# Optimization experiments

Measured on AMD Instinct MI355X. Metric: run time of the kernel, lower is better.

The kernel has to match this reference:

```python
import jax, jax.numpy as jnp
import numpy as np
from jax import lax


def ternarize(w):
    """Standard TWN ternarization with straight-through estimator.
    delta = 0.7*mean(|w|); alpha = mean(|w|) over kept entries; w_t = alpha*sign(w)*mask.
    """
    a = jnp.abs(w)
    delta = 0.7 * a.mean()
    mask = (a > delta).astype(w.dtype)
    alpha = (a * mask).sum() / jnp.maximum(mask.sum(), 1.0)
    wt = alpha * jnp.sign(w) * mask
    return w + lax.stop_gradient(wt - w)  # STE


def conv3x3(x, w, b):
    y = lax.conv_general_dilated(x, ternarize(w), window_strides=(1, 1),
                                 padding=((1, 1), (1, 1)),
                                 dimension_numbers=('NCHW', 'OIHW', 'NCHW'))
    return y + b[None, :, None, None]


def maxpool2(x):
    return lax.reduce_window(x, -jnp.inf, lax.max, (1, 1, 2, 2), (1, 1, 2, 2), 'VALID')


def setup_inputs() -> dict:
    key = jax.random.key(0)
    ks = jax.random.split(key, 11)
    s = lambda k, shape, scale: jax.random.normal(k, shape, dtype=jnp.float32) * scale
    return {
        'x':   s(ks[0], (1024, 3, 32, 32), 1.0),
        'w1':  s(ks[1], (64, 3, 3, 3), 0.1),
        'b1':  s(ks[2], (64,), 0.01),
        'w2':  s(ks[3], (128, 64, 3, 3), 0.05),
        'b2':  s(ks[4], (128,), 0.01),
        'w3':  s(ks[5], (256, 128, 3, 3), 0.03),
        'b3':  s(ks[6], (256,), 0.01),
        'wf1': s(ks[7], (256, 4096), 0.02),
        'bf1': s(ks[8], (256,), 0.01),
        'wf2': s(ks[9], (10, 256), 0.06),
        'bf2': s(ks[10], (10,), 0.01),
    }


def reference(x, w1, b1, w2, b2, w3, b3, wf1, bf1, wf2, bf2):
    x = maxpool2(jax.nn.relu(conv3x3(x, w1, b1)))   # [B,64,16,16]
    x = maxpool2(jax.nn.relu(conv3x3(x, w2, b2)))   # [B,128,8,8]
    x = maxpool2(jax.nn.relu(conv3x3(x, w3, b3)))   # [B,256,4,4]
    x = x.reshape(-1, 256 * 4 * 4)
    x = jax.nn.relu(x @ ternarize(wf1).T + bf1)     # [B,256]
    return x @ ternarize(wf2).T + bf2               # [B,10]
```

## Files before the change

kernel.cpp:

```cpp
#include <hip/hip_runtime.h>
#include <hip/hip_bf16.h>


typedef __attribute__((ext_vector_type(8))) short short8;
typedef __attribute__((ext_vector_type(4))) float f32x4;
typedef __attribute__((ext_vector_type(4))) int i32x4;

__device__ __forceinline__ unsigned short f2bf(float x) {
    unsigned u = __float_as_uint(x);
    return (unsigned short)((u + 0x7fffu + ((u >> 16) & 1u)) >> 16);
}
__device__ __forceinline__ float bf2f(unsigned short b) {
    return __uint_as_float(((unsigned)b) << 16);
}

#define WS_W1B   0
#define N_W1B    2048
#define WS_W2P   (WS_W1B + N_W1B)
#define N_W2P    (9*128*64)
#define WS_W3P   (WS_W2P + N_W2P)
#define N_W3P    (9*256*128)
#define WS_WTF1  (WS_W3P + N_W3P)
#define N_WTF1   (256*4096)
#define WS_WTF2  (WS_WTF1 + N_WTF1)
#define N_WTF2   (10*256)
#define WS_A1    (WS_WTF2 + N_WTF2)
#define N_A1     (1024*256*64)
#define WS_A2    (WS_A1 + N_A1)
#define N_A2     (1024*64*128)
#define WS_A3    (WS_A2 + N_A2)
#define N_A3     (1024*16*256)
#define WS_F1    (WS_A3 + N_A3)
#define N_F1     (1024*256)
#define WS_SCR   (WS_F1 + N_F1)

#define FC1_S    16

struct TernArgs {
    const float* w[6];
    int n[6];
};

__global__ void tern_stats1(TernArgs ta, double* __restrict__ scr) {
    const int wi = blockIdx.y;
    const float* __restrict__ w = ta.w[wi];
    const int n = ta.n[wi];
    __shared__ double red[4];
    const int lane = threadIdx.x & 63, wv = threadIdx.x >> 6;
    if (wi == 5) {
        float m = 0.f;
        for (int i = blockIdx.x * blockDim.x + threadIdx.x; i < n;
             i += gridDim.x * blockDim.x)
            m = fmaxf(m, fabsf(w[i]));
        #pragma unroll
        for (int off = 32; off > 0; off >>= 1)
            m = fmaxf(m, __shfl_down(m, off, 64));
        if (lane == 0) red[wv] = (double)m;
        __syncthreads();
        if (threadIdx.x == 0) {
            float mm = (float)fmax(fmax(red[0], red[1]), fmax(red[2], red[3]));
            atomicMax((int*)(scr + 20), __float_as_int(mm));
        }
        return;
    }
    double s = 0.0;
    for (int i = blockIdx.x * blockDim.x + threadIdx.x; i < n;
         i += gridDim.x * blockDim.x)
        s += (double)fabsf(w[i]);
    #pragma unroll
    for (int off = 32; off > 0; off >>= 1) s += __shfl_down(s, off, 64);
    if (lane == 0) red[wv] = s;
    __syncthreads();
    if (threadIdx.x == 0)
        atomicAdd(scr + wi * 4, red[0] + red[1] + red[2] + red[3]);
}

__global__ void tern_stats2(TernArgs ta, double* __restrict__ scr) {
    const int wi = blockIdx.y;
    const float* __restrict__ w = ta.w[wi];
    const int n = ta.n[wi];
    const float delta = (float)(0.7 * scr[wi * 4] / (double)n);
    double ms = 0.0, cnt = 0.0;
    for (int i = blockIdx.x * blockDim.x + threadIdx.x; i < n;
         i += gridDim.x * blockDim.x) {
        float a = fabsf(w[i]);
        if (a > delta) { ms += (double)a; cnt += 1.0; }
    }
    #pragma unroll
    for (int off = 32; off > 0; off >>= 1) {
        ms += __shfl_down(ms, off, 64);
        cnt += __shfl_down(cnt, off, 64);
    }
    __shared__ double redm[4], redc[4];
    const int lane = threadIdx.x & 63, wv = threadIdx.x >> 6;
    if (lane == 0) { redm[wv] = ms; redc[wv] = cnt; }
    __syncthreads();
    if (threadIdx.x == 0) {
        atomicAdd(scr + wi * 4 + 1, redm[0] + redm[1] + redm[2] + redm[3]);
        atomicAdd(scr + wi * 4 + 2, redc[0] + redc[1] + redc[2] + redc[3]);
    }
}

__global__ void tern_write_all(TernArgs ta, const double* __restrict__ scr,
                               signed char* __restrict__ w1b,
                               signed char* __restrict__ w2p8,
                               signed char* __restrict__ w3p8,
                               unsigned short* __restrict__ wtf1b,
                               float* __restrict__ wtf2) {
    const int wi = blockIdx.y;
    const float* __restrict__ w = ta.w[wi];
    const int n = ta.n[wi];
    const double* sc = scr + wi * 4;
    const float delta = (float)(0.7 * sc[0] / (double)n);
    const int i0 = blockIdx.x * blockDim.x + threadIdx.x;
    const int stride = gridDim.x * blockDim.x;

    if (wi == 0) {
        for (int i = i0; i < n; i += stride) {
            const int co = i / 27;
            const int kp = i % 27;
            float v = w[i];
            signed char s = (fabsf(v) > delta) ? (v > 0.0f ? 1 : -1) : 0;
            w1b[co * 64 + kp] = s;
            w1b[4096 + co * 64 + 32 + kp] = s;
        }
    } else if (wi == 4) {
        const double c = sc[2];
        const float alpha = (float)(sc[1] / (c > 1.0 ? c : 1.0));
        for (int i = i0; i < n; i += stride) {
            float v = w[i];
            wtf2[i] = (fabsf(v) > delta) ? (v > 0.0f ? alpha : -alpha) : 0.0f;
        }
    } else if (wi == 1 || wi == 2) {
        const int CIc = (wi == 1) ? 64 : 128;
        const int COc = (wi == 1) ? 128 : 256;
        signed char* dst = (wi == 1) ? w2p8 : w3p8;
        for (int i = i0; i < n; i += stride) {
            const int co = i / (CIc * 9);
            const int r = i % (CIc * 9);
            const int ci = r / 9, tap = r % 9;
            float v = w[i];
            signed char s = (fabsf(v) > delta) ? (v > 0.0f ? 1 : -1) : 0;
            dst[(tap * COc + co) * CIc + ci] = s;
        }
    } else {
        for (int i = i0; i < n; i += stride) {
            const int j = i >> 12;
            const int k = i & 4095;
            const int c = k >> 4, px = k & 15;
            float v = w[i];
            unsigned short s = (fabsf(v) > delta) ? (v > 0.0f ? 0x3f80 : 0xbf80) : 0;
            unsigned short* row = wtf1b + ((long)j << 13) + px * 512 + c;
            row[0] = s;
            row[256] = s;
        }
    }
}

__global__ __launch_bounds__(256) void conv1_i8(
        const float* __restrict__ x,
        const signed char* __restrict__ w1b,
        const float* __restrict__ bias,
        const double* __restrict__ scr,
        const int* __restrict__ amax_x,
        int* __restrict__ amax_out,
        float* __restrict__ y) {
    constexpr int PL = 3472;
    __shared__ __align__(16) char X[2 * PL];
    __shared__ float redm[4];

    const int b = blockIdx.x;
    const int tid = threadIdx.x;
    const float S = 32512.0f / fmaxf(__int_as_float(*amax_x), 1e-30f);

    for (int i = tid; i < 2 * PL / 16; i += 256)
        ((int4*)X)[i] = make_int4(0, 0, 0, 0);
    __syncthreads();

    for (int i = tid; i < 768; i += 256) {
        const float4 v = ((const float4*)(x + (long)b * 3072))[i];
        const int e = i * 4;
        const int ci = e >> 10;
        const int rem = e & 1023;
        const int h = rem >> 5, w = rem & 31;
        const int base = ci * 1156 + (h + 1) * 34 + (w + 1);
        const float f[4] = {v.x, v.y, v.z, v.w};
        #pragma unroll
        for (int j = 0; j < 4; j++) {
            const int q = __float2int_rn(f[j] * S);
            const int ql = (q << 24) >> 24;
            const int qh = (q - ql) >> 8;
            X[base + j] = (char)ql;
            X[PL + base + j] = (char)qh;
        }
    }
    __syncthreads();

    const int lane = tid & 63;
    const int wid = tid >> 6;
    const int lm = lane & 15;
    const int kg = lane >> 4;

    const int poff = (kg >= 2) ? PL : 0;
    int cst[16];
    #pragma unroll
    for (int j = 0; j < 16; j++) {
        const int kp = (kg & 1) * 16 + j;
        cst[j] = (kp < 27)
                     ? ((kp / 9) * 1156 + ((kp % 9) / 3) * 34 + (kp % 9) % 3)
                     : 0;
    }

    i32x4 BL[4], BH[4];
    #pragma unroll
    for (int nt = 0; nt < 4; nt++) {
        const int co = nt * 16 + lm;
        BL[nt] = *(const i32x4*)(w1b + (long)co * 64 + kg * 16);
        BH[nt] = *(const i32x4*)(w1b + 4096 + (long)co * 64 + kg * 16);
    }

    const double c2 = scr[2];
    const float alpha = (float)(scr[1] / (c2 > 1.0 ? c2 : 1.0));
    const float dq = alpha / S;
    float tmax = 0.f;
    float* yb = y + (long)b * 256 * 64;

    for (int tt = 0; tt < 16; ++tt) {
        const int t = wid * 16 + tt;
        const int pp = t * 4 + (lm >> 2);
        const int sub = lm & 3;
        const int h = 2 * (pp >> 4) + (sub >> 1);
        const int w = 2 * (pp & 15) + (sub & 1);
        const int base = poff + h * 34 + w;
        unsigned d[4] = {0u, 0u, 0u, 0u};
        #pragma unroll
        for (int j = 0; j < 16; j++) {
            const unsigned byte = (unsigned char)X[base + cst[j]];
            d[j >> 2] |= byte << ((j & 3) * 8);
        }
        i32x4 Af;
        Af[0] = (int)d[0]; Af[1] = (int)d[1];
        Af[2] = (int)d[2]; Af[3] = (int)d[3];

        const int opp = t * 4 + kg;
        float* yr = yb + (long)opp * 64;
        #pragma unroll
        for (int nt = 0; nt < 4; nt++) {
            i32x4 aL = 0, aH = 0;
            aL = __builtin_amdgcn_mfma_i32_16x16x64_i8(Af, BL[nt], aL, 0, 0, 0);
            aH = __builtin_amdgcn_mfma_i32_16x16x64_i8(Af, BH[nt], aH, 0, 0, 0);
            const int s0 = aH[0] * 256 + aL[0];
            const int s1 = aH[1] * 256 + aL[1];
            const int s2 = aH[2] * 256 + aL[2];
            const int s3 = aH[3] * 256 + aL[3];
            int sm = s0 > s1 ? s0 : s1;
            const int sn = s2 > s3 ? s2 : s3;
            sm = sm > sn ? sm : sn;
            const int co = nt * 16 + lm;
            const float o = fmaxf(dq * (float)sm + bias[co], 0.f);
            tmax = fmaxf(tmax, o);
            yr[co] = o;
        }
    }

    #pragma unroll
    for (int off = 32; off > 0; off >>= 1)
        tmax = fmaxf(tmax, __shfl_down(tmax, off, 64));
    if (lane == 0) redm[wid] = tmax;
    __syncthreads();
    if (tid == 0) {
        float m = fmaxf(fmaxf(redm[0], redm[1]), fmaxf(redm[2], redm[3]));
        atomicMax(amax_out, __float_as_int(m));
    }
}

template <int CI, int HI, int CO, int HB, int WM, int WN, bool INF32>
__global__ __launch_bounds__(256) void conv_i8(
        const void* __restrict__ xin,
        const signed char* __restrict__ wp,
        const float* __restrict__ bias,
        const double* __restrict__ scr,
        const int* __restrict__ amax_in,
        int* __restrict__ amax_out,
        unsigned short* __restrict__ yout) {
    constexpr int CH8 = CI / 64;
    constexpr int NITER = 9 * CH8;
    constexpr int HR = HI / HB;
    constexpr int ROWS = HR + 2;
    constexpr int COLS = HI + 2;
    constexpr int NPIX = ROWS * COLS;
    constexpr int PSTR = NPIX * 64 + 32;
    constexpr int PO = HI / 2;
    constexpr int POR = HR / 2;
    constexpr int MT = 4, NT = 4;
    constexpr int NST = ROWS * HI * (CI / 8) / 256;
    static_assert(WM * WN == 4, "4 waves");
    static_assert(WM * 64 == HR * HI, "M covers slab pixels");
    static_assert(WN * 64 == CO, "N covers all co");
    static_assert(NST * 256 == ROWS * HI * (CI / 8), "exact staging trips");

    __shared__ __align__(16) char X[2 * CH8 * PSTR];
    __shared__ float redm[4];

    const int bimg = blockIdx.x / HB;
    const int hb = blockIdx.x % HB;
    const int tid = threadIdx.x;

    const float S = 32512.0f / fmaxf(__int_as_float(*amax_in), 1e-30f);

    constexpr int HALO = 2 * COLS + 2 * (ROWS - 2);
    for (int i = tid; i < HALO * 2 * CH8 * 4; i += 256) {
        const int u = i & 3;
        const int t = i >> 2;
        const int g = t % (2 * CH8);
        const int hp = t / (2 * CH8);
        int p;
        if (hp < COLS) p = hp;
        else if (hp < 2 * COLS) p = (ROWS - 1) * COLS + (hp - COLS);
        else {
            const int e = hp - 2 * COLS;
            p = (1 + (e >> 1)) * COLS + ((e & 1) ? (COLS - 1) : 0);
        }
        *(int4*)&X[g * PSTR + p * 64 + u * 16] = make_int4(0, 0, 0, 0);
    }

    uint4 va[NST], vb[NST];
    bool val[NST];
    int pidx[NST], cbase[NST];
    #pragma unroll
    for (int s2 = 0; s2 < NST; s2++) {
        const int i = tid + s2 * 256;
        const int q8 = i % (CI / 8);
        const int t = i / (CI / 8);
        const int c = t % HI;
        const int r = t / HI;
        const int h = hb * HR + r - 1;
        val[s2] = (unsigned)h < (unsigned)HI;
        pidx[s2] = r * COLS + c + 1;
        cbase[s2] = q8 * 8;
        if (val[s2]) {
            if (INF32) {
                const float* pxr = (const float*)xin +
                    ((long)(bimg * HI + h) * HI + c) * CI + q8 * 8;
                va[s2] = *(const uint4*)(pxr);
                vb[s2] = *(const uint4*)(pxr + 4);
            } else {
                const unsigned short* pxr = (const unsigned short*)xin +
                    ((long)(bimg * HI + h) * HI + c) * (2 * CI);
                va[s2] = *(const uint4*)(pxr + q8 * 8);
                vb[s2] = *(const uint4*)(pxr + CI + q8 * 8);
            }
        }
    }
    #pragma unroll
    for (int s2 = 0; s2 < NST; s2++) {
        if (!val[s2]) continue;
        float f[8];
        if (INF32) {
            const float* fa = (const float*)&va[s2];
            const float* fb = (const float*)&vb[s2];
            #pragma unroll
            for (int j = 0; j < 4; j++) { f[j] = fa[j]; f[4 + j] = fb[j]; }
        } else {
            const unsigned* hw = (const unsigned*)&va[s2];
            const unsigned* lw = (const unsigned*)&vb[s2];
            #pragma unroll
            for (int j = 0; j < 8; j++) {
                const unsigned hu = (j & 1) ? (hw[j >> 1] >> 16)
                                            : (hw[j >> 1] & 0xffffu);
                const unsigned lu = (j & 1) ? (lw[j >> 1] >> 16)
                                            : (lw[j >> 1] & 0xffffu);
                f[j] = __uint_as_float(hu << 16) + __uint_as_float(lu << 16);
            }
        }
        unsigned pl0 = 0, pl1 = 0, ph0 = 0, ph1 = 0;
        #pragma unroll
        for (int j = 0; j < 8; j++) {
            const int qi = (int)(f[j] * S + 0.5f);
            const int ql = (qi << 24) >> 24;
            const int qh = (qi - ql) >> 8;
            const int sh = (j & 3) * 8;
            if (j < 4) {
                pl0 |= (unsigned)(ql & 255) << sh;
                ph0 |= (unsigned)(qh & 255) << sh;
            } else {
                pl1 |= (unsigned)(ql & 255) << sh;
                ph1 |= (unsigned)(qh & 255) << sh;
            }
        }
        const int p = pidx[s2];
        const int ch = cbase[s2] >> 6;
        const int cc = cbase[s2] & 63;
        const int slot = ((cc >> 4) + (p >> 1)) & 3;
        const int base = p * 64 + slot * 16 + (cc & 15);
        *(uint2*)&X[ch * PSTR + base] = make_uint2(pl0, pl1);
        *(uint2*)&X[(CH8 + ch) * PSTR + base] = make_uint2(ph0, ph1);
    }
    __syncthreads();

    const int lane = tid & 63;
    const int wid = tid >> 6;
    const int wm = (WM == 1) ? 0 : (wid >> 1);
    const int wn = (WM == 1) ? wid : (wid & 1);
    const int lm = lane & 15;
    const int kg = lane >> 4;

    int pb[MT];
    #pragma unroll
    for (int mt = 0; mt < MT; mt++) {
        const int m = (wm * MT + mt) * 16 + lm;
        const int pp = m >> 2, sub = m & 3;
        const int lph = pp / PO, lpw = pp % PO;
        const int h = 2 * lph + (sub >> 1);
        const int w = 2 * lpw + (sub & 1);
        pb[mt] = h * COLS + w;
    }
    const signed char* bp[NT];
    #pragma unroll
    for (int nt = 0; nt < NT; nt++) {
        const int co = (wn * NT + nt) * 16 + lm;
        bp[nt] = wp + (long)co * CI + kg * 16;
    }

    i32x4 accL[MT][NT], accH[MT][NT];
    #pragma unroll
    for (int mt = 0; mt < MT; mt++)
        #pragma unroll
        for (int nt = 0; nt < NT; nt++) { accL[mt][nt] = 0; accH[mt][nt] = 0; }

    i32x4 Bb[2][NT];
    #pragma unroll
    for (int nt = 0; nt < NT; nt++) Bb[0][nt] = *(const i32x4*)(bp[nt]);

    #pragma unroll 2
    for (int it = 0; it < NITER; ++it) {
        const int cur = it & 1, nxt = cur ^ 1;
        if (it + 1 < NITER) {
            const int it1 = it + 1;
            const int tap = it1 / CH8, ch1 = it1 % CH8;
            const int woff = tap * CO * CI + ch1 * 64;
            #pragma unroll
            for (int nt = 0; nt < NT; nt++)
                Bb[nxt][nt] = *(const i32x4*)(bp[nt] + woff);
        }
        const int tap = it / CH8, ch = it % CH8;
        const int dtap = (tap / 3) * COLS + (tap % 3);
        i32x4 Af0[MT], Af1[MT];
        #pragma unroll
        for (int mt = 0; mt < MT; mt++) {
            const int p = pb[mt] + dtap;
            const int ao = p * 64 + (((kg + (p >> 1)) & 3) << 4);
            Af0[mt] = *(const i32x4*)&X[ch * PSTR + ao];
            Af1[mt] = *(const i32x4*)&X[(CH8 + ch) * PSTR + ao];
        }
        #pragma unroll
        for (int mt = 0; mt < MT; mt++)
            #pragma unroll
            for (int nt = 0; nt < NT; nt++)
                accL[mt][nt] = __builtin_amdgcn_mfma_i32_16x16x64_i8(
                    Af0[mt], Bb[cur][nt], accL[mt][nt], 0, 0, 0);
        #pragma unroll
        for (int mt = 0; mt < MT; mt++)
            #pragma unroll
            for (int nt = 0; nt < NT; nt++)
                accH[mt][nt] = __builtin_amdgcn_mfma_i32_16x16x64_i8(
                    Af1[mt], Bb[cur][nt], accH[mt][nt], 0, 0, 0);
    }

    const double c2 = scr[2];
    const float alpha = (float)(scr[1] / (c2 > 1.0 ? c2 : 1.0));
    const float dq = alpha / S;
    float tmax = 0.f;
    #pragma unroll
    for (int mt = 0; mt < MT; mt++) {
        const int pp = (wm * MT + mt) * 4 + kg;
        const int lph = pp / PO, lpw = pp % PO;
        const int gpp = (hb * POR + lph) * PO + lpw;
        unsigned short* yr = yout + ((long)bimg * (PO * PO) + gpp) * (2 * CO);
        #pragma unroll
        for (int nt = 0; nt < NT; nt++) {
            const int co = (wn * NT + nt) * 16 + lm;
            const i32x4 aL = accL[mt][nt], aH = accH[mt][nt];
            int s0 = aH[0] * 256 + aL[0];
            int s1 = aH[1] * 256 + aL[1];
            int s2 = aH[2] * 256 + aL[2];
            int s3 = aH[3] * 256 + aL[3];
            int sm = s0 > s1 ? s0 : s1;
            int sn = s2 > s3 ? s2 : s3;
            sm = sm > sn ? sm : sn;
            float o = fmaxf(dq * (float)sm + bias[co], 0.f);
            tmax = fmaxf(tmax, o);
            unsigned short hi = f2bf(o);
            unsigned short lo = f2bf(o - bf2f(hi));
            yr[co] = hi;
            yr[CO + co] = lo;
        }
    }
    if (amax_out) {
        #pragma unroll
        for (int off = 32; off > 0; off >>= 1)
            tmax = fmaxf(tmax, __shfl_down(tmax, off, 64));
        if (lane == 0) redm[wid] = tmax;
        __syncthreads();
        if (tid == 0) {
            float m = fmaxf(fmaxf(redm[0], redm[1]), fmaxf(redm[2], redm[3]));
            atomicMax(amax_out, __float_as_int(m));
        }
    }
}

template <int S>
__global__ __launch_bounds__(256) void fc1_mfma(
        const unsigned short* __restrict__ A,
        const unsigned short* __restrict__ Bw,
        float* __restrict__ parts) {
    constexpr int KCH = 8192 / S;
    constexpr int NSTEP = KCH / 32;
    const int m0 = blockIdx.x * 128;
    const int n0 = blockIdx.y * 128;
    const int s = blockIdx.z;
    const int tid = threadIdx.x;
    const int lane = tid & 63, wid = tid >> 6;
    const int wm = wid >> 1, wn = wid & 1;
    const int lm = lane & 15, kg = lane >> 4;

    const long k0 = (long)s * KCH + kg * 8;
    const unsigned short* ap[4];
    const unsigned short* bp[4];
    #pragma unroll
    for (int t = 0; t < 4; t++) {
        ap[t] = A + (long)(m0 + wm * 64 + t * 16 + lm) * 8192 + k0;
        bp[t] = Bw + (long)(n0 + wn * 64 + t * 16 + lm) * 8192 + k0;
    }

    f32x4 acc[4][4] = {};
    short8 Ab[2][4], Bb[2][4];
    #pragma unroll
    for (int t = 0; t < 4; t++) {
        Ab[0][t] = *(const short8*)(ap[t]);
        Bb[0][t] = *(const short8*)(bp[t]);
    }

    #pragma unroll 2
    for (int st = 0; st < NSTEP; ++st) {
        const int cur = st & 1, nxt = cur ^ 1;
        if (st + 1 < NSTEP) {
            const int off = (st + 1) * 32;
            #pragma unroll
            for (int t = 0; t < 4; t++) {
                Ab[nxt][t] = *(const short8*)(ap[t] + off);
                Bb[nxt][t] = *(const short8*)(bp[t] + off);
            }
        }
        #pragma unroll
        for (int mt = 0; mt < 4; mt++)
            #pragma unroll
            for (int nt = 0; nt < 4; nt++)
                acc[mt][nt] = __builtin_amdgcn_mfma_f32_16x16x32_bf16(
                    Ab[cur][mt], Bb[cur][nt], acc[mt][nt], 0, 0, 0);
    }

    #pragma unroll
    for (int mt = 0; mt < 4; mt++) {
        #pragma unroll
        for (int r = 0; r < 4; r++) {
            const int b = m0 + wm * 64 + mt * 16 + kg * 4 + r;
            #pragma unroll
            for (int nt = 0; nt < 4; nt++) {
                const int j = n0 + wn * 64 + nt * 16 + lm;
                parts[((long)s * 1024 + b) * 256 + j] = acc[mt][nt][r];
            }
        }
    }
}

template <int S>
__global__ void fc1_reduce(const float* __restrict__ parts,
                           const double* __restrict__ scr,
                           const float* __restrict__ bias,
                           float* __restrict__ f1) {
    const int idx = blockIdx.x * blockDim.x + threadIdx.x;
    const int j = idx & 255;
    float s = 0.f;
    #pragma unroll
    for (int p = 0; p < S; p++) s += parts[(long)p * 262144 + idx];
    const double c2 = scr[2];
    const float alpha = (float)(scr[1] / (c2 > 1.0 ? c2 : 1.0));
    f1[idx] = fmaxf(alpha * s + bias[j], 0.f);
}

__global__ void fc2_kernel(const float* __restrict__ a,
                           const float* __restrict__ wt,
                           const float* __restrict__ bias,
                           float* __restrict__ out, int B) {
    const int idx = blockIdx.x * blockDim.x + threadIdx.x;
    if (idx >= B * 10) return;
    const int k = idx % 10;
    const int b = idx / 10;
    const float* ar = a + (long)b * 256;
    const float* wr = wt + (long)k * 256;
    float acc = 0.f;
    #pragma unroll 4
    for (int i = 0; i < 256; i++) acc += ar[i] * wr[i];
    out[idx] = acc + bias[k];
}

extern "C" void kernel_launch(void* const* d_in, const int* in_sizes, int n_in,
                              void* d_out, int out_size, void* d_ws, size_t ws_size,
                              hipStream_t stream) {
    const float* x   = (const float*)d_in[0];
    const float* w1  = (const float*)d_in[1];
    const float* b1  = (const float*)d_in[2];
    const float* w2  = (const float*)d_in[3];
    const float* b2  = (const float*)d_in[4];
    const float* w3  = (const float*)d_in[5];
    const float* b3  = (const float*)d_in[6];
    const float* wf1 = (const float*)d_in[7];
    const float* bf1 = (const float*)d_in[8];
    const float* wf2 = (const float*)d_in[9];
    const float* bf2 = (const float*)d_in[10];
    float* out = (float*)d_out;
    float* ws = (float*)d_ws;

    const int B = 1024;

    signed char*    w1b   = (signed char*)(ws + WS_W1B);
    signed char*    w2p8  = (signed char*)(ws + WS_W2P);
    signed char*    w3p8  = (signed char*)(ws + WS_W3P);
    unsigned short* wtf1b = (unsigned short*)(ws + WS_WTF1);
    float*          wtf2  = ws + WS_WTF2;
    float*          a1f   = ws + WS_A1;
    unsigned short* a2p   = (unsigned short*)(ws + WS_A2);
    unsigned short* a3p   = (unsigned short*)(ws + WS_A3);
    float*          f1    = ws + WS_F1;
    double*         scr   = (double*)(ws + WS_SCR);
    int*            iscr  = (int*)(scr + 20);
    int*            amaxx = iscr;
    int*            amax1 = iscr + 1;
    int*            amax2 = iscr + 2;
    float*          parts = ws + WS_A1;

    hipMemsetAsync(scr, 0, 22 * sizeof(double), stream);
    hipMemsetAsync(w1b, 0, 8192, stream);

    TernArgs ta;
    ta.w[0] = w1;  ta.n[0] = 64 * 27;
    ta.w[1] = w2;  ta.n[1] = 128 * 64 * 9;
    ta.w[2] = w3;  ta.n[2] = 256 * 128 * 9;
    ta.w[3] = wf1; ta.n[3] = 256 * 4096;
    ta.w[4] = wf2; ta.n[4] = 10 * 256;
    ta.w[5] = x;   ta.n[5] = 1024 * 3 * 32 * 32;

    hipLaunchKernelGGL(tern_stats1, dim3(128, 6), dim3(256), 0, stream, ta, scr);
    hipLaunchKernelGGL(tern_stats2, dim3(128, 5), dim3(256), 0, stream, ta, scr);
    hipLaunchKernelGGL(tern_write_all, dim3(128, 5), dim3(256), 0, stream,
                       ta, scr, w1b, w2p8, w3p8, wtf1b, wtf2);

    hipLaunchKernelGGL(conv1_i8, dim3(B), dim3(256), 0, stream,
                       x, w1b, b1, scr + 0, amaxx, amax1, a1f);

    hipLaunchKernelGGL((conv_i8<64, 16, 128, 2, 2, 2, true>), dim3(B * 2),
                       dim3(256), 0, stream, a1f, w2p8, b2, scr + 4, amax1,
                       amax2, a2p);

    hipLaunchKernelGGL((conv_i8<128, 8, 256, 1, 1, 4, false>), dim3(B),
                       dim3(256), 0, stream, a2p, w3p8, b3, scr + 8, amax2,
                       (int*)nullptr, a3p);

    hipLaunchKernelGGL((fc1_mfma<FC1_S>), dim3(8, 2, FC1_S), dim3(256), 0, stream,
                       a3p, wtf1b, parts);
    hipLaunchKernelGGL((fc1_reduce<FC1_S>), dim3(1024), dim3(256), 0, stream,
                       parts, scr + 12, bf1, f1);

    hipLaunchKernelGGL(fc2_kernel, dim3((B * 10 + 255) / 256), dim3(256), 0,
                       stream, f1, wtf2, bf2, out, B);
}
```

Measured before the change: 307.8 us.

## Cut conv register pressure for two blocks per CU and fuse fc1 reduce with fc2

The conv_i8 kernel now requests two resident blocks per CU through launch bounds. To fit that register budget, its input staging becomes a simple strided loop that no longer holds every load in registers, and the MFMA loop loads the low-half and high-half A fragments in two separate phases. Separately, the fc1 partial-sum reduction, ReLU and fc2 are fused into one per-image kernel that keeps the fc1 activations in shared memory and reduces with wave shuffles. The trade-off is less memory-latency hiding during staging, and possible register spills if the tighter bound cannot be met.

Result: faster. 285.5 us (-7.2%).

```diff
diff --git a/kernel.cpp b/kernel.cpp
--- a/kernel.cpp
+++ b/kernel.cpp
@@ -275,7 +275,7 @@
 }
 
 template <int CI, int HI, int CO, int HB, int WM, int WN, bool INF32>
-__global__ __launch_bounds__(256) void conv_i8(
+__global__ __launch_bounds__(256, 2) void conv_i8(
         const void* __restrict__ xin,
         const signed char* __restrict__ wp,
         const float* __restrict__ bias,
@@ -293,11 +293,9 @@
     constexpr int PO = HI / 2;
     constexpr int POR = HR / 2;
     constexpr int MT = 4, NT = 4;
-    constexpr int NST = ROWS * HI * (CI / 8) / 256;
     static_assert(WM * WN == 4, "4 waves");
     static_assert(WM * 64 == HR * HI, "M covers slab pixels");
     static_assert(WN * 64 == CO, "N covers all co");
-    static_assert(NST * 256 == ROWS * HI * (CI / 8), "exact staging trips");
 
     __shared__ __align__(16) char X[2 * CH8 * PSTR];
     __shared__ float redm[4];
@@ -324,46 +322,28 @@
         *(int4*)&X[g * PSTR + p * 64 + u * 16] = make_int4(0, 0, 0, 0);
     }
 
-    uint4 va[NST], vb[NST];
-    bool val[NST];
-    int pidx[NST], cbase[NST];
-    #pragma unroll
-    for (int s2 = 0; s2 < NST; s2++) {
-        const int i = tid + s2 * 256;
+    for (int i = tid; i < ROWS * HI * (CI / 8); i += 256) {
         const int q8 = i % (CI / 8);
         const int t = i / (CI / 8);
         const int c = t % HI;
         const int r = t / HI;
         const int h = hb * HR + r - 1;
-        val[s2] = (unsigned)h < (unsigned)HI;
-        pidx[s2] = r * COLS + c + 1;
-        cbase[s2] = q8 * 8;
-        if (val[s2]) {
-            if (INF32) {
-                const float* pxr = (const float*)xin +
-                    ((long)(bimg * HI + h) * HI + c) * CI + q8 * 8;
-                va[s2] = *(const uint4*)(pxr);
-                vb[s2] = *(const uint4*)(pxr + 4);
-            } else {
-                const unsigned short* pxr = (const unsigned short*)xin +
-                    ((long)(bimg * HI + h) * HI + c) * (2 * CI);
-                va[s2] = *(const uint4*)(pxr + q8 * 8);
-                vb[s2] = *(const uint4*)(pxr + CI + q8 * 8);
-            }
-        }
-    }
-    #pragma unroll
-    for (int s2 = 0; s2 < NST; s2++) {
-        if (!val[s2]) continue;
+        if ((unsigned)h >= (unsigned)HI) continue;
         float f[8];
         if (INF32) {
-            const float* fa = (const float*)&va[s2];
-            const float* fb = (const float*)&vb[s2];
-            #pragma unroll
-            for (int j = 0; j < 4; j++) { f[j] = fa[j]; f[4 + j] = fb[j]; }
+            const float* pxr = (const float*)xin +
+                ((long)(bimg * HI + h) * HI + c) * CI + q8 * 8;
+            const float4 va = *(const float4*)(pxr);
+            const float4 vb = *(const float4*)(pxr + 4);
+            f[0] = va.x; f[1] = va.y; f[2] = va.z; f[3] = va.w;
+            f[4] = vb.x; f[5] = vb.y; f[6] = vb.z; f[7] = vb.w;
         } else {
-            const unsigned* hw = (const unsigned*)&va[s2];
-            const unsigned* lw = (const unsigned*)&vb[s2];
+            const unsigned short* pxr = (const unsigned short*)xin +
+                ((long)(bimg * HI + h) * HI + c) * (2 * CI);
+            const uint4 vh = *(const uint4*)(pxr + q8 * 8);
+            const uint4 vl = *(const uint4*)(pxr + CI + q8 * 8);
+            const unsigned* hw = (const unsigned*)&vh;
+            const unsigned* lw = (const unsigned*)&vl;
             #pragma unroll
             for (int j = 0; j < 8; j++) {
                 const unsigned hu = (j & 1) ? (hw[j >> 1] >> 16)
@@ -388,9 +368,9 @@
                 ph1 |= (unsigned)(qh & 255) << sh;
             }
         }
-        const int p = pidx[s2];
-        const int ch = cbase[s2] >> 6;
-        const int cc = cbase[s2] & 63;
+        const int p = r * COLS + c + 1;
+        const int ch = q8 >> 3;
+        const int cc = (q8 * 8) & 63;
         const int slot = ((cc >> 4) + (p >> 1)) & 3;
         const int base = p * 64 + slot * 16 + (cc & 15);
         *(uint2*)&X[ch * PSTR + base] = make_uint2(pl0, pl1);
@@ -445,26 +425,36 @@
         }
         const int tap = it / CH8, ch = it % CH8;
         const int dtap = (tap / 3) * COLS + (tap % 3);
-        i32x4 Af0[MT], Af1[MT];
+        int ao[MT];
         #pragma unroll
         for (int mt = 0; mt < MT; mt++) {
             const int p = pb[mt] + dtap;
-            const int ao = p * 64 + (((kg + (p >> 1)) & 3) << 4);
-            Af0[mt] = *(const i32x4*)&X[ch * PSTR + ao];
-            Af1[mt] = *(const i32x4*)&X[(CH8 + ch) * PSTR + ao];
-        }
-        #pragma unroll
-        for (int mt = 0; mt < MT; mt++)
-            #pragma unroll
-            for (int nt = 0; nt < NT; nt++)
-                accL[mt][nt] = __builtin_amdgcn_mfma_i32_16x16x64_i8(
-                    Af0[mt], Bb[cur][nt], accL[mt][nt], 0, 0, 0);
-        #pragma unroll
-        for (int mt = 0; mt < MT; mt++)
-            #pragma unroll
-            for (int nt = 0; nt < NT; nt++)
-                accH[mt][nt] = __builtin_amdgcn_mfma_i32_16x16x64_i8(
-                    Af1[mt], Bb[cur][nt], accH[mt][nt], 0, 0, 0);
+            ao[mt] = p * 64 + (((kg + (p >> 1)) & 3) << 4);
+        }
+        {
+            i32x4 Af[MT];
+            #pragma unroll
+            for (int mt = 0; mt < MT; mt++)
+                Af[mt] = *(const i32x4*)&X[ch * PSTR + ao[mt]];
+            #pragma unroll
+            for (int mt = 0; mt < MT; mt++)
+                #pragma unroll
+                for (int nt = 0; nt < NT; nt++)
+                    accL[mt][nt] = __builtin_amdgcn_mfma_i32_16x16x64_i8(
+                        Af[mt], Bb[cur][nt], accL[mt][nt], 0, 0, 0);
+        }
+        {
+            i32x4 Af[MT];
+            #pragma unroll
+            for (int mt = 0; mt < MT; mt++)
+                Af[mt] = *(const i32x4*)&X[(CH8 + ch) * PSTR + ao[mt]];
+            #pragma unroll
+            for (int mt = 0; mt < MT; mt++)
+                #pragma unroll
+                for (int nt = 0; nt < NT; nt++)
+                    accH[mt][nt] = __builtin_amdgcn_mfma_i32_16x16x64_i8(
+                        Af[mt], Bb[cur][nt], accH[mt][nt], 0, 0, 0);
+        }
     }
 
     const double c2 = scr[2];
@@ -575,34 +565,36 @@
 }
 
 template <int S>
-__global__ void fc1_reduce(const float* __restrict__ parts,
-                           const double* __restrict__ scr,
-                           const float* __restrict__ bias,
-                           float* __restrict__ f1) {
-    const int idx = blockIdx.x * blockDim.x + threadIdx.x;
-    const int j = idx & 255;
+__global__ __launch_bounds__(256) void fc2_fused(
+        const float* __restrict__ parts,
+        const double* __restrict__ scr,
+        const float* __restrict__ bf1v,
+        const float* __restrict__ wtf2,
+        const float* __restrict__ bf2v,
+        float* __restrict__ out) {
+    __shared__ float sf[256];
+    const int b = blockIdx.x;
+    const int j = threadIdx.x;
     float s = 0.f;
     #pragma unroll
-    for (int p = 0; p < S; p++) s += parts[(long)p * 262144 + idx];
+    for (int p = 0; p < S; p++)
+        s += parts[(long)p * 262144 + (long)b * 256 + j];
     const double c2 = scr[2];
     const float alpha = (float)(scr[1] / (c2 > 1.0 ? c2 : 1.0));
-    f1[idx] = fmaxf(alpha * s + bias[j], 0.f);
-}
-
-__global__ void fc2_kernel(const float* __restrict__ a,
-                           const float* __restrict__ wt,
-                           const float* __restrict__ bias,
-                           float* __restrict__ out, int B) {
-    const int idx = blockIdx.x * blockDim.x + threadIdx.x;
-    if (idx >= B * 10) return;
-    const int k = idx % 10;
-    const int b = idx / 10;
-    const float* ar = a + (long)b * 256;
-    const float* wr = wt + (long)k * 256;
-    float acc = 0.f;
-    #pragma unroll 4
-    for (int i = 0; i < 256; i++) acc += ar[i] * wr[i];
-    out[idx] = acc + bias[k];
+    sf[j] = fmaxf(alpha * s + bf1v[j], 0.f);
+    __syncthreads();
+    const int lane = threadIdx.x & 63, wid = threadIdx.x >> 6;
+    for (int k = wid; k < 10; k += 4) {
+        const float* wr = wtf2 + k * 256;
+        float acc = 0.f;
+        #pragma unroll
+        for (int t = 0; t < 4; t++)
+            acc += sf[lane + t * 64] * wr[lane + t * 64];
+        #pragma unroll
+        for (int off = 32; off > 0; off >>= 1)
+            acc += __shfl_down(acc, off, 64);
+        if (lane == 0) out[(long)b * 10 + k] = acc + bf2v[k];
+    }
 }
 
 extern "C" void kernel_launch(void* const* d_in, const int* in_sizes, int n_in,
@@ -632,7 +624,6 @@
     float*          a1f   = ws + WS_A1;
     unsigned short* a2p   = (unsigned short*)(ws + WS_A2);
     unsigned short* a3p   = (unsigned short*)(ws + WS_A3);
-    float*          f1    = ws + WS_F1;
     double*         scr   = (double*)(ws + WS_SCR);
     int*            iscr  = (int*)(scr + 20);
     int*            amaxx = iscr;
@@ -669,9 +660,7 @@
 
     hipLaunchKernelGGL((fc1_mfma<FC1_S>), dim3(8, 2, FC1_S), dim3(256), 0, stream,
                        a3p, wtf1b, parts);
-    hipLaunchKernelGGL((fc1_reduce<FC1_S>), dim3(1024), dim3(256), 0, stream,
-                       parts, scr + 12, bf1, f1);
-
-    hipLaunchKernelGGL(fc2_kernel, dim3((B * 10 + 255) / 256), dim3(256), 0,
-                       stream, f1, wtf2, bf2, out, B);
-}
+
+    hipLaunchKernelGGL((fc2_fused<FC1_S>), dim3(B), dim3(256), 0, stream,
+                       parts, scr + 12, bf1, wtf2, bf2, out);
+}
```
